# Performance work log

Hardware: AMD Instinct MI355X
Metric: run time of the kernel (lower is better)

The kernel has to match this reference:

```python
import jax, jax.numpy as jnp
import numpy as np

D_MODEL = 1024
D_STATE = 16
D_CONV = 4
EXPAND = 2
DT_RANK = 64
D_INNER = EXPAND * D_MODEL
B, L = 1, 2048


def setup_inputs() -> dict:
    key = jax.random.key(0)
    ks = jax.random.split(key, 10)
    x = jax.random.normal(ks[0], (B, L, D_MODEL), dtype=jnp.float32)
    # linear weights (stored as [out, in], like torch)
    W_in = jax.random.normal(ks[1], (2 * D_INNER, D_MODEL), dtype=jnp.float32) * (1.0 / np.sqrt(D_MODEL))
    conv_w = jax.random.normal(ks[2], (D_INNER, 1, D_CONV), dtype=jnp.float32) * (1.0 / np.sqrt(D_CONV))
    conv_b = jax.random.normal(ks[3], (D_INNER,), dtype=jnp.float32) * 0.02
    W_x = jax.random.normal(ks[4], (DT_RANK + 2 * D_STATE, D_INNER), dtype=jnp.float32) * (1.0 / np.sqrt(D_INNER))
    W_dt = jax.random.normal(ks[5], (D_INNER, DT_RANK), dtype=jnp.float32) * (1.0 / np.sqrt(DT_RANK))
    # dt bias init: inverse-softplus of dt ~ LogUniform(1e-3, 0.1)
    dt = jnp.exp(jax.random.uniform(ks[6], (D_INNER,)) * (np.log(0.1) - np.log(0.001)) + np.log(0.001))
    dt = jnp.clip(dt, 1e-4, None)
    b_dt = dt + jnp.log(-jnp.expm1(-dt))
    # A_log init: log(1..d_state) broadcast over d_inner
    A_log = jnp.log(jnp.broadcast_to(jnp.arange(1, D_STATE + 1, dtype=jnp.float32)[None, :], (D_INNER, D_STATE)))
    D_param = jnp.ones((D_INNER,), dtype=jnp.float32)
    W_out = jax.random.normal(ks[7], (D_MODEL, D_INNER), dtype=jnp.float32) * (1.0 / np.sqrt(D_INNER))
    return dict(x=x, W_in=W_in, conv_w=conv_w, conv_b=conv_b, W_x=W_x,
                W_dt=W_dt, b_dt=b_dt, A_log=A_log, D_param=D_param, W_out=W_out)


def _silu(v):
    return v * jax.nn.sigmoid(v)


def _mamba_forward(x, W_in, conv_w, conv_b, W_x, W_dt, b_dt, A_log, D_param, W_out):
    # in_proj: (B, L, 2*d_inner)
    xz = jnp.einsum('bld,ed->ble', x, W_in)
    x_in, z = jnp.split(xz, 2, axis=-1)  # each (B, L, d_inner)

    # depthwise causal conv1d (torch pads d_conv-1 both sides then truncates -> causal left pad)
    xc = jnp.transpose(x_in, (0, 2, 1))  # (B, d_inner, L)
    xc = jax.lax.conv_general_dilated(
        xc, conv_w,
        window_strides=(1,), padding=[(D_CONV - 1, 0)],
        dimension_numbers=('NCH', 'OIH', 'NCH'),
        feature_group_count=D_INNER)
    xc = xc + conv_b[None, :, None]
    x_conv = _silu(jnp.transpose(xc, (0, 2, 1)))  # (B, L, d_inner)

    # selective SSM
    A = -jnp.exp(A_log)  # (d_inner, d_state)
    x_dbl = jnp.einsum('bld,ed->ble', x_conv, W_x)  # (B, L, dt_rank + 2*d_state)
    dt_low, B_ssm, C = jnp.split(x_dbl, [DT_RANK, DT_RANK + D_STATE], axis=-1)
    dt = jax.nn.softplus(jnp.einsum('blr,dr->bld', dt_low, W_dt) + b_dt)  # (B, L, d_inner)

    dA = jnp.exp(jnp.einsum('bld,dn->bldn', dt, A))                        # (B, L, d_inner, d_state)
    dBx = dt[..., None] * B_ssm[:, :, None, :] * x_conv[..., None]          # dB * x, (B, L, d_inner, d_state)

    def step(h, inp):
        dA_t, dBx_t, C_t = inp          # (B, d, n), (B, d, n), (B, n)
        h = dA_t * h + dBx_t
        y_t = jnp.einsum('bdn,bn->bd', h, C_t)
        return h, y_t

    h0 = jnp.zeros((x.shape[0], D_INNER, D_STATE), dtype=x.dtype)
    xs = (jnp.swapaxes(dA, 0, 1), jnp.swapaxes(dBx, 0, 1), jnp.swapaxes(C, 0, 1))
    _, ys = jax.lax.scan(step, h0, xs)   # ys: (L, B, d_inner)
    y = jnp.swapaxes(ys, 0, 1) + x_conv * D_param  # (B, L, d_inner)

    y = y * _silu(z)
    return jnp.einsum('bld,ed->ble', y, W_out)  # (B, L, d_model)


def reference(x, W_in, conv_w, conv_b, W_x, W_dt, b_dt, A_log, D_param, W_out):
    return _mamba_forward(x, W_in, conv_w, conv_b, W_x, W_dt, b_dt, A_log, D_param, W_out)
```

## Files before the change

### kernel.cpp

```cpp
#include <hip/hip_runtime.h>
#include <math.h>

#define LSEQ   2048
#define DMODEL 1024
#define DINNER 2048
#define DSTATE 16
#define DTRANK 64
#define XCOLS  96
#define CL     32
#define NC     (LSEQ/CL)
#define SSTATE (DINNER*DSTATE)

typedef __attribute__((ext_vector_type(8))) short bf16x8;
typedef __attribute__((ext_vector_type(4))) float f32x4;
typedef unsigned short ushort_t;
typedef unsigned int uint_t;

__device__ __forceinline__ float siluf(float v) { return v / (1.f + __expf(-v)); }

__device__ __forceinline__ ushort_t f2bf(float f) {
    uint_t u = __float_as_uint(f);
    u += 0x7FFFu + ((u >> 16) & 1u);
    return (ushort_t)(u >> 16);
}
__device__ __forceinline__ float bf2f(ushort_t u) {
    return __uint_as_float((uint_t)u << 16);
}

__device__ __forceinline__ bf16x8 cvt8(float4 lo, float4 hi) {
    bf16x8 r;
    r[0] = (short)f2bf(lo.x); r[1] = (short)f2bf(lo.y);
    r[2] = (short)f2bf(lo.z); r[3] = (short)f2bf(lo.w);
    r[4] = (short)f2bf(hi.x); r[5] = (short)f2bf(hi.y);
    r[6] = (short)f2bf(hi.z); r[7] = (short)f2bf(hi.w);
    return r;
}

__global__ __launch_bounds__(256)
void cast6_kernel(const float* __restrict__ s0, ushort_t* __restrict__ d0, int c0,
                  const float* __restrict__ s1, ushort_t* __restrict__ d1, int c1,
                  const float* __restrict__ s2, ushort_t* __restrict__ d2, int c2,
                  const float* __restrict__ s3, ushort_t* __restrict__ d3, int c3,
                  const float* __restrict__ s4, ushort_t* __restrict__ d4, int c4,
                  float* __restrict__ z0, int cz)
{
    int i = (blockIdx.x * 256 + threadIdx.x) * 8;
    int tot = c0 + c1 + c2 + c3 + c4;
    if (i < tot) {
        const float* s; ushort_t* d;
        if (i < c0)                { s = s0 + i;                  d = d0 + i; }
        else if (i < c0+c1)        { s = s1 + (i-c0);             d = d1 + (i-c0); }
        else if (i < c0+c1+c2)     { s = s2 + (i-c0-c1);          d = d2 + (i-c0-c1); }
        else if (i < c0+c1+c2+c3)  { s = s3 + (i-c0-c1-c2);       d = d3 + (i-c0-c1-c2); }
        else                       { s = s4 + (i-c0-c1-c2-c3);    d = d4 + (i-c0-c1-c2-c3); }
        *(bf16x8*)d = cvt8(*(const float4*)s, *(const float4*)(s + 4));
    } else if (i < tot + cz) {
        float* z = z0 + (i - tot);
        *(float4*)z       = make_float4(0.f, 0.f, 0.f, 0.f);
        *(float4*)(z + 4) = make_float4(0.f, 0.f, 0.f, 0.f);
    }
}

__device__ __forceinline__ void stage_tile(const ushort_t* __restrict__ A,
                                           const ushort_t* __restrict__ B,
                                           ushort_t* As, ushort_t* Bs,
                                           int m0, int n0, int K, int k0, int tid)
{
#pragma unroll
    for (int j = 0; j < 2; j++) {
        const int c   = j * 256 + tid;
        const int row = c & 127;
        const int kbi = c >> 7;
        __builtin_amdgcn_global_load_lds(
            (const __attribute__((address_space(1))) uint_t*)(A + (size_t)(m0 + row) * K + k0 + kbi * 8),
            (__attribute__((address_space(3))) uint_t*)((char*)As + c * 16), 16, 0, 0);
        __builtin_amdgcn_global_load_lds(
            (const __attribute__((address_space(1))) uint_t*)(B + (size_t)(n0 + row) * K + k0 + kbi * 8),
            (__attribute__((address_space(3))) uint_t*)((char*)Bs + c * 16), 16, 0, 0);
    }
}

template<int EPI, int SPLITK>
__global__ __launch_bounds__(256)
void gemm_bf16(const ushort_t* __restrict__ A,
               const ushort_t* __restrict__ B,
               float* __restrict__ C,
               ushort_t* __restrict__ Xb,
               ushort_t* __restrict__ Gz,
               int M, int N, int K, size_t partStride)
{
    __shared__ ushort_t As[2][4096];
    __shared__ ushort_t Bs[2][4096];

    const int tid  = threadIdx.x;
    const int wid  = tid >> 6;
    const int lane = tid & 63;
    const int m0 = blockIdx.x * 128;
    const int n0 = blockIdx.y * 128;
    const int kcnt  = K / SPLITK;
    const int kbase = (SPLITK > 1) ? blockIdx.z * kcnt : 0;
    const int NT = kcnt / 32;
    float* Cp = (EPI == 0) ? C + (size_t)blockIdx.z * partStride : C;
    const int wr = (wid >> 1) * 64;
    const int wc = (wid & 1) * 64;
    const int lr = lane & 15;
    const int kbq = lane >> 4;

    f32x4 acc[4][4];
#pragma unroll
    for (int m = 0; m < 4; m++)
#pragma unroll
        for (int n = 0; n < 4; n++)
            acc[m][n] = (f32x4){0.f, 0.f, 0.f, 0.f};

    stage_tile(A, B, As[0], Bs[0], m0, n0, K, kbase, tid);

    for (int t = 0; t < NT; t++) {
        const int cur = t & 1;
        if (t + 1 < NT) {
            stage_tile(A, B, As[cur ^ 1], Bs[cur ^ 1], m0, n0, K, kbase + (t + 1) * 32, tid);
            asm volatile("s_waitcnt vmcnt(4)" ::: "memory");
        } else {
            asm volatile("s_waitcnt vmcnt(0)" ::: "memory");
        }
        __builtin_amdgcn_s_barrier();
        __builtin_amdgcn_sched_barrier(0);

        bf16x8 af[4], bfr[4];
#pragma unroll
        for (int m = 0; m < 4; m++)
            af[m] = *(const bf16x8*)&As[cur][(kbq * 128 + wr + m * 16 + lr) * 8];
#pragma unroll
        for (int n = 0; n < 4; n++)
            bfr[n] = *(const bf16x8*)&Bs[cur][(kbq * 128 + wc + n * 16 + lr) * 8];
#pragma unroll
        for (int m = 0; m < 4; m++)
#pragma unroll
            for (int n = 0; n < 4; n++)
                acc[m][n] = __builtin_amdgcn_mfma_f32_16x16x32_bf16(af[m], bfr[n], acc[m][n], 0, 0, 0);

        __builtin_amdgcn_sched_barrier(0);
        __builtin_amdgcn_s_barrier();
    }

    const int er = (lane >> 4) * 4;
    const int ec = lane & 15;
    if (EPI == 0) {
#pragma unroll
        for (int m = 0; m < 4; m++) {
            const int grow = m0 + wr + m * 16 + er;
#pragma unroll
            for (int n = 0; n < 4; n++) {
                const int gcol = n0 + wc + n * 16 + ec;
#pragma unroll
                for (int r = 0; r < 4; r++)
                    Cp[(size_t)(grow + r) * N + gcol] = acc[m][n][r];
            }
        }
    } else {
        const bool xside = (n0 < DINNER);
        ushort_t* eps = (wid < 2) ? As[wid] : Bs[wid - 2];
#pragma unroll
        for (int m = 0; m < 4; m++)
#pragma unroll
            for (int n = 0; n < 4; n++)
#pragma unroll
                for (int r = 0; r < 4; r++) {
                    const int rl = m * 16 + er + r;
                    const int cl = n * 16 + ec;
                    float v = acc[m][n][r];
                    eps[rl * 64 + (cl ^ ((rl & 7) * 8))] =
                        xside ? f2bf(v) : f2bf(siluf(v));
                }
        __syncthreads();
        const int row8 = lane >> 3;
        const int c8   = (lane & 7) * 8;
#pragma unroll
        for (int p = 0; p < 8; p++) {
            const int rl = p * 8 + row8;
            bf16x8 v = *(const bf16x8*)&eps[rl * 64 + (c8 ^ ((rl & 7) * 8))];
            const int grow = m0 + wr + rl;
            const int gcol = n0 + wc + c8;
            if (xside)
                *(bf16x8*)(Xb + (size_t)grow * DINNER + gcol) = v;
            else
                *(bf16x8*)(Gz + (size_t)grow * DINNER + (gcol - DINNER)) = v;
        }
    }
}

__global__ __launch_bounds__(256)
void add2_kernel(const float* __restrict__ p0, const float* __restrict__ p1,
                 float* __restrict__ out, int n)
{
    int i = (blockIdx.x * 256 + threadIdx.x) * 4;
    if (i >= n) return;
    float4 a = *(const float4*)(p0 + i);
    float4 b = *(const float4*)(p1 + i);
    *(float4*)(out + i) = make_float4(a.x + b.x, a.y + b.y, a.z + b.z, a.w + b.w);
}

__global__ __launch_bounds__(256)
void gemm_xdbl(const ushort_t* __restrict__ A,
               const ushort_t* __restrict__ B,
               float* __restrict__ Cout)
{
    const int tid = threadIdx.x, wid = tid >> 6, lane = tid & 63;
    const int m0 = blockIdx.x * 128;
    const int kbase = blockIdx.z * 128;
    const int wr = (wid >> 1) * 64;
    const int wc = (wid & 1) * 48;
    const int lr = lane & 15;
    const int kq = (lane >> 4) * 8;

    f32x4 acc[4][3];
#pragma unroll
    for (int m = 0; m < 4; m++)
#pragma unroll
        for (int n = 0; n < 3; n++)
            acc[m][n] = (f32x4){0.f, 0.f, 0.f, 0.f};

#pragma unroll
    for (int ks = 0; ks < 4; ks++) {
        const int k0 = kbase + ks * 32;
        bf16x8 af[4], bfr[3];
#pragma unroll
        for (int m = 0; m < 4; m++)
            af[m] = *(const bf16x8*)(A + (size_t)(m0 + wr + m * 16 + lr) * DINNER + k0 + kq);
#pragma unroll
        for (int n = 0; n < 3; n++)
            bfr[n] = *(const bf16x8*)(B + (size_t)(wc + n * 16 + lr) * DINNER + k0 + kq);
#pragma unroll
        for (int m = 0; m < 4; m++)
#pragma unroll
            for (int n = 0; n < 3; n++)
                acc[m][n] = __builtin_amdgcn_mfma_f32_16x16x32_bf16(af[m], bfr[n], acc[m][n], 0, 0, 0);
    }

    const int er = (lane >> 4) * 4;
    const int ec = lane & 15;
#pragma unroll
    for (int m = 0; m < 4; m++)
#pragma unroll
        for (int n = 0; n < 3; n++)
#pragma unroll
            for (int r = 0; r < 4; r++)
                atomicAdd(&Cout[(size_t)(m0 + wr + m * 16 + er + r) * XCOLS + wc + n * 16 + ec],
                          acc[m][n][r]);
}

__global__ __launch_bounds__(256)
void gemm_dt(const float* __restrict__ Axd,
             const ushort_t* __restrict__ Bw,
             const float* __restrict__ bias,
             ushort_t* __restrict__ dtmb)
{
    __shared__ ushort_t eps4[4][4096];
    const int tid = threadIdx.x, wid = tid >> 6, lane = tid & 63;
    const int m0 = blockIdx.x * 128;
    const int n0 = blockIdx.y * 128;
    const int wr = (wid >> 1) * 64;
    const int wc = (wid & 1) * 64;
    const int lr = lane & 15;
    const int kq = (lane >> 4) * 8;

    f32x4 acc[4][4];
#pragma unroll
    for (int m = 0; m < 4; m++)
#pragma unroll
        for (int n = 0; n < 4; n++)
            acc[m][n] = (f32x4){0.f, 0.f, 0.f, 0.f};

#pragma unroll
    for (int kk = 0; kk < 2; kk++) {
        bf16x8 af[4], bfr[4];
#pragma unroll
        for (int m = 0; m < 4; m++) {
            const float* p = Axd + (size_t)(m0 + wr + m * 16 + lr) * XCOLS + kk * 32 + kq;
            af[m] = cvt8(*(const float4*)p, *(const float4*)(p + 4));
        }
#pragma unroll
        for (int n = 0; n < 4; n++)
            bfr[n] = *(const bf16x8*)(Bw + (size_t)(n0 + wc + n * 16 + lr) * DTRANK + kk * 32 + kq);
#pragma unroll
        for (int m = 0; m < 4; m++)
#pragma unroll
            for (int n = 0; n < 4; n++)
                acc[m][n] = __builtin_amdgcn_mfma_f32_16x16x32_bf16(af[m], bfr[n], acc[m][n], 0, 0, 0);
    }

    const int er = (lane >> 4) * 4;
    const int ec = lane & 15;
    ushort_t* eps = eps4[wid];
#pragma unroll
    for (int m = 0; m < 4; m++)
#pragma unroll
        for (int n = 0; n < 4; n++) {
            const int cl = n * 16 + ec;
            const float bv = bias[n0 + wc + cl];
#pragma unroll
            for (int r = 0; r < 4; r++) {
                const int rl = m * 16 + er + r;
                float c = acc[m][n][r] + bv;
                c = (c > 20.f) ? c : log1pf(__expf(c));
                eps[rl * 64 + (cl ^ ((rl & 7) * 8))] = f2bf(c);
            }
        }
    __syncthreads();
    const int row8 = lane >> 3;
    const int c8   = (lane & 7) * 8;
#pragma unroll
    for (int p = 0; p < 8; p++) {
        const int rl = p * 8 + row8;
        bf16x8 v = *(const bf16x8*)&eps[rl * 64 + (c8 ^ ((rl & 7) * 8))];
        dtmb[(size_t)(m0 + wr + rl) * DINNER + n0 + wc + c8] = 0;
        *(bf16x8*)(dtmb + (size_t)(m0 + wr + rl) * DINNER + n0 + wc + c8) = v;
    }
}

__global__ __launch_bounds__(256)
void conv_silu_kernel(const ushort_t* __restrict__ xinb,
                      const float* __restrict__ conv_w,
                      const float* __restrict__ conv_b,
                      ushort_t* __restrict__ xcb)
{
    int idx = blockIdx.x * 256 + threadIdx.x;
    if (idx >= LSEQ * DINNER) return;
    int t = idx / DINNER;
    int d = idx - t * DINNER;
    float acc = conv_b[d];
#pragma unroll
    for (int j = 0; j < 4; j++) {
        int tt = t - 3 + j;
        if (tt >= 0)
            acc = fmaf(conv_w[d*4 + j], bf2f(xinb[(size_t)tt * DINNER + d]), acc);
    }
    xcb[idx] = f2bf(siluf(acc));
}

__global__ __launch_bounds__(256)
void scan_phase1(const ushort_t* __restrict__ dtmb,
                 const float* __restrict__ xdbl,
                 const ushort_t* __restrict__ xcb,
                 const float* __restrict__ A_log,
                 float2* __restrict__ state)
{
    __shared__ float Bs[CL][16];
    const int tid = threadIdx.x;
    const int d = blockIdx.x * 256 + tid;
    const int c = blockIdx.y;
    const int t0 = c * CL;

    {
        int t = tid >> 3, n = (tid * 2) & 15;
        float2 v = *(const float2*)&xdbl[(size_t)(t0 + t) * XCOLS + DTRANK + n];
        Bs[t][n] = v.x; Bs[t][n + 1] = v.y;
    }

    float a[16];
#pragma unroll
    for (int q = 0; q < 4; q++) {
        f32x4 v = *(const f32x4*)&A_log[(size_t)d * DSTATE + q * 4];
#pragma unroll
        for (int j = 0; j < 4; j++) a[q * 4 + j] = -__expf(v[j]);
    }
    float h[16];
#pragma unroll
    for (int n = 0; n < 16; n++) h[n] = 0.f;
    float sdt = 0.f;

    __syncthreads();

    float dtv = bf2f(dtmb[(size_t)t0 * DINNER + d]);
    float xv  = bf2f(xcb[(size_t)t0 * DINNER + d]);
    for (int tt = 0; tt < CL; tt++) {
        int tn_ = t0 + ((tt + 1 < CL) ? tt + 1 : tt);
        float dtv_n = bf2f(dtmb[(size_t)tn_ * DINNER + d]);
        float xv_n  = bf2f(xcb[(size_t)tn_ * DINNER + d]);

        f32x4 Bq[4];
#pragma unroll
        for (int q = 0; q < 4; q++) Bq[q] = *(const f32x4*)&Bs[tt][q * 4];
        float dtx = dtv * xv;
        sdt += dtv;
#pragma unroll
        for (int n = 0; n < 16; n++) {
            float e = __expf(dtv * a[n]);
            h[n] = fmaf(e, h[n], dtx * Bq[n >> 2][n & 3]);
        }
        dtv = dtv_n; xv = xv_n;
    }

#pragma unroll
    for (int n = 0; n < 16; n++)
        state[(size_t)c * SSTATE + (size_t)n * DINNER + d] =
            make_float2(__expf(a[n] * sdt), h[n]);
}

__global__ __launch_bounds__(256)
void scan_phase2(float2* __restrict__ state)
{
    const int idx = blockIdx.x * 256 + threadIdx.x;
    float carry = 0.f;
#pragma unroll
    for (int c = 0; c < NC; c++) {
        float2 s = state[(size_t)c * SSTATE + idx];
        ((float*)&state[(size_t)c * SSTATE + idx])[1] = carry;
        carry = fmaf(s.x, carry, s.y);
    }
}

__global__ __launch_bounds__(256)
void scan_phase3(const ushort_t* __restrict__ dtmb,
                 const float* __restrict__ xdbl,
                 const ushort_t* __restrict__ xcb,
                 const float* __restrict__ A_log,
                 const float* __restrict__ Dp,
                 const ushort_t* __restrict__ gz,
                 const float2* __restrict__ state,
                 ushort_t* __restrict__ yb)
{
    __shared__ float Bs[CL][16];
    __shared__ float Cs[CL][16];
    const int tid = threadIdx.x;
    const int d = blockIdx.x * 256 + tid;
    const int c = blockIdx.y;
    const int t0 = c * CL;

    {
        int r = tid & 127;
        int t = r >> 2, n = (r * 4) & 15;
        const float* src = &xdbl[(size_t)(t0 + t) * XCOLS + DTRANK + ((tid < 128) ? 0 : DSTATE) + n];
        float4 v = *(const float4*)src;
        float* dst = (tid < 128) ? &Bs[t][n] : &Cs[t][n];
        dst[0] = v.x; dst[1] = v.y; dst[2] = v.z; dst[3] = v.w;
    }

    float a[16];
#pragma unroll
    for (int q = 0; q < 4; q++) {
        f32x4 v = *(const f32x4*)&A_log[(size_t)d * DSTATE + q * 4];
#pragma unroll
        for (int j = 0; j < 4; j++) a[q * 4 + j] = -__expf(v[j]);
    }
    const float Dv = Dp[d];
    float h[16];
#pragma unroll
    for (int n = 0; n < 16; n++)
        h[n] = state[(size_t)c * SSTATE + (size_t)n * DINNER + d].y;

    __syncthreads();

    float dtv = bf2f(dtmb[(size_t)t0 * DINNER + d]);
    float xv  = bf2f(xcb[(size_t)t0 * DINNER + d]);
    for (int tt = 0; tt < CL; tt++) {
        const int t = t0 + tt;
        int tn_ = t0 + ((tt + 1 < CL) ? tt + 1 : tt);
        float dtv_n = bf2f(dtmb[(size_t)tn_ * DINNER + d]);
        float xv_n  = bf2f(xcb[(size_t)tn_ * DINNER + d]);
        float gzv   = bf2f(gz[(size_t)t * DINNER + d]);

        f32x4 Bq[4], Cq[4];
#pragma unroll
        for (int q = 0; q < 4; q++) {
            Bq[q] = *(const f32x4*)&Bs[tt][q * 4];
            Cq[q] = *(const f32x4*)&Cs[tt][q * 4];
        }
        float dtx = dtv * xv;
        float y = 0.f;
#pragma unroll
        for (int n = 0; n < 16; n++) {
            float e = __expf(dtv * a[n]);
            h[n] = fmaf(e, h[n], dtx * Bq[n >> 2][n & 3]);
            y = fmaf(h[n], Cq[n >> 2][n & 3], y);
        }
        yb[(size_t)t * DINNER + d] = f2bf((y + Dv * xv) * gzv);
        dtv = dtv_n; xv = xv_n;
    }
}

extern "C" void kernel_launch(void* const* d_in, const int* in_sizes, int n_in,
                              void* d_out, int out_size, void* d_ws, size_t ws_size,
                              hipStream_t stream)
{
    const float* x      = (const float*)d_in[0];
    const float* W_in   = (const float*)d_in[1];
    const float* conv_w = (const float*)d_in[2];
    const float* conv_b = (const float*)d_in[3];
    const float* W_x    = (const float*)d_in[4];
    const float* W_dt   = (const float*)d_in[5];
    const float* b_dt   = (const float*)d_in[6];
    const float* A_log  = (const float*)d_in[7];
    const float* D_par  = (const float*)d_in[8];
    const float* W_out  = (const float*)d_in[9];
    float* out = (float*)d_out;
    float* ws  = (float*)d_ws;

    float*  xdbl  = ws;
    float2* state = (float2*)(xdbl + (size_t)LSEQ * XCOLS);
    ushort_t* xb   = (ushort_t*)(state + (size_t)NC * SSTATE);
    ushort_t* Wib  = xb   + (size_t)LSEQ * DMODEL;
    ushort_t* Wob  = Wib  + (size_t)(2*DINNER) * DMODEL;
    ushort_t* Wxb  = Wob  + (size_t)DMODEL * DINNER;
    ushort_t* Wdtb = Wxb  + (size_t)XCOLS * DINNER;
    ushort_t* xinb = Wdtb + (size_t)DINNER * DTRANK;
    ushort_t* gz   = xinb + (size_t)LSEQ * DINNER;
    ushort_t* xcb  = gz   + (size_t)LSEQ * DINNER;
    ushort_t* dtmb = xcb  + (size_t)LSEQ * DINNER;
    ushort_t* yb   = dtmb + (size_t)LSEQ * DINNER;
    float* outp = (float*)xinb;

    {
        int c0 = LSEQ * DMODEL, c1 = 2 * DINNER * DMODEL, c2 = DMODEL * DINNER;
        int c3 = XCOLS * DINNER, c4 = DINNER * DTRANK;
        int cz = LSEQ * XCOLS;
        int total = c0 + c1 + c2 + c3 + c4 + cz;
        hipLaunchKernelGGL(cast6_kernel, dim3((total / 8 + 255) / 256), dim3(256), 0, stream,
                           x, xb, c0, W_in, Wib, c1, W_out, Wob, c2,
                           W_x, Wxb, c3, W_dt, Wdtb, c4, xdbl, cz);
    }

    hipLaunchKernelGGL((gemm_bf16<1,1>), dim3(LSEQ/128, (2*DINNER)/128), dim3(256), 0, stream,
                       xb, Wib, (float*)nullptr, xinb, gz, LSEQ, 2*DINNER, DMODEL, (size_t)0);

    hipLaunchKernelGGL(conv_silu_kernel, dim3((LSEQ*DINNER)/256), dim3(256), 0, stream,
                       xinb, conv_w, conv_b, xcb);

    hipLaunchKernelGGL(gemm_xdbl, dim3(LSEQ/128, 1, 16), dim3(256), 0, stream,
                       xcb, Wxb, xdbl);

    hipLaunchKernelGGL(gemm_dt, dim3(LSEQ/128, DINNER/128), dim3(256), 0, stream,
                       xdbl, Wdtb, b_dt, dtmb);

    hipLaunchKernelGGL(scan_phase1, dim3(DINNER/256, NC), dim3(256), 0, stream,
                       dtmb, xdbl, xcb, A_log, state);
    hipLaunchKernelGGL(scan_phase2, dim3(SSTATE/256), dim3(256), 0, stream,
                       state);
    hipLaunchKernelGGL(scan_phase3, dim3(DINNER/256, NC), dim3(256), 0, stream,
                       dtmb, xdbl, xcb, A_log, D_par, gz, state, yb);

    hipLaunchKernelGGL((gemm_bf16<0,2>), dim3(LSEQ/128, DMODEL/128, 2), dim3(256), 0, stream,
                       yb, Wob, outp, (ushort_t*)nullptr, (ushort_t*)nullptr,
                       LSEQ, DMODEL, DINNER, (size_t)(LSEQ*DMODEL));
    hipLaunchKernelGGL(add2_kernel, dim3((LSEQ*DMODEL/4)/256), dim3(256), 0, stream,
                       outp, outp + (size_t)LSEQ*DMODEL, out, LSEQ*DMODEL);
}
```

Measured before the change: 203.3 us.

## Use 256x256-tile 512-thread GEMM for in_proj and drop redundant dt store

```diff
diff --git a/kernel.cpp b/kernel.cpp
--- a/kernel.cpp
+++ b/kernel.cpp
@@ -61,6 +61,120 @@
     }
 }
 
+__device__ __forceinline__ void stage256(const ushort_t* __restrict__ A,
+                                         const ushort_t* __restrict__ B,
+                                         ushort_t* LDS, int buf,
+                                         int m0, int n0, int k0, int tid)
+{
+    ushort_t* As = LDS + buf * 16384;
+    ushort_t* Bs = LDS + 32768 + buf * 16384;
+#pragma unroll
+    for (int j = 0; j < 4; j++) {
+        const int c   = j * 512 + tid;
+        const int row = c & 255;
+        const int kb  = c >> 8;
+        __builtin_amdgcn_global_load_lds(
+            (const __attribute__((address_space(1))) uint_t*)(A + (size_t)(m0 + row) * DMODEL + k0 + kb * 8),
+            (__attribute__((address_space(3))) uint_t*)((char*)As + c * 16), 16, 0, 0);
+        __builtin_amdgcn_global_load_lds(
+            (const __attribute__((address_space(1))) uint_t*)(B + (size_t)(n0 + row) * DMODEL + k0 + kb * 8),
+            (__attribute__((address_space(3))) uint_t*)((char*)Bs + c * 16), 16, 0, 0);
+    }
+}
+
+__global__ __launch_bounds__(512)
+void gemm256_inproj(const ushort_t* __restrict__ A,
+                    const ushort_t* __restrict__ B,
+                    ushort_t* __restrict__ Xb,
+                    ushort_t* __restrict__ Gz)
+{
+    __shared__ ushort_t LDS[65536];
+
+    const int tid  = threadIdx.x;
+    const int wid  = tid >> 6;
+    const int lane = tid & 63;
+    const int m0 = blockIdx.x * 256;
+    const int n0 = blockIdx.y * 256;
+    const int NT = DMODEL / 64;
+    const int wr = (wid >> 2) * 128;
+    const int wc = (wid & 3) * 64;
+    const int lr = lane & 15;
+    const int kq = lane >> 4;
+
+    f32x4 acc[8][4];
+#pragma unroll
+    for (int m = 0; m < 8; m++)
+#pragma unroll
+        for (int n = 0; n < 4; n++)
+            acc[m][n] = (f32x4){0.f, 0.f, 0.f, 0.f};
+
+    stage256(A, B, LDS, 0, m0, n0, 0, tid);
+
+    for (int t = 0; t < NT; t++) {
+        const int cur = t & 1;
+        if (t + 1 < NT) {
+            stage256(A, B, LDS, cur ^ 1, m0, n0, (t + 1) * 64, tid);
+            asm volatile("s_waitcnt vmcnt(8)" ::: "memory");
+        } else {
+            asm volatile("s_waitcnt vmcnt(0)" ::: "memory");
+        }
+        __builtin_amdgcn_s_barrier();
+        __builtin_amdgcn_sched_barrier(0);
+
+        const ushort_t* Asc = LDS + cur * 16384;
+        const ushort_t* Bsc = LDS + 32768 + cur * 16384;
+
+        bf16x8 bfr[2][4];
+#pragma unroll
+        for (int kk = 0; kk < 2; kk++)
+#pragma unroll
+            for (int n = 0; n < 4; n++)
+                bfr[kk][n] = *(const bf16x8*)&Bsc[((kk * 4 + kq) * 256 + wc + n * 16 + lr) * 8];
+#pragma unroll
+        for (int m = 0; m < 8; m++) {
+            bf16x8 af0 = *(const bf16x8*)&Asc[((0 * 4 + kq) * 256 + wr + m * 16 + lr) * 8];
+            bf16x8 af1 = *(const bf16x8*)&Asc[((1 * 4 + kq) * 256 + wr + m * 16 + lr) * 8];
+#pragma unroll
+            for (int n = 0; n < 4; n++) {
+                acc[m][n] = __builtin_amdgcn_mfma_f32_16x16x32_bf16(af0, bfr[0][n], acc[m][n], 0, 0, 0);
+                acc[m][n] = __builtin_amdgcn_mfma_f32_16x16x32_bf16(af1, bfr[1][n], acc[m][n], 0, 0, 0);
+            }
+        }
+
+        __builtin_amdgcn_sched_barrier(0);
+        __builtin_amdgcn_s_barrier();
+    }
+
+    const bool xside = (n0 < DINNER);
+    ushort_t* eps = LDS + wid * 8192;
+    const int er = (lane >> 4) * 4;
+    const int ec = lane & 15;
+#pragma unroll
+    for (int m = 0; m < 8; m++)
+#pragma unroll
+        for (int n = 0; n < 4; n++)
+#pragma unroll
+            for (int r = 0; r < 4; r++) {
+                const int rl = m * 16 + er + r;
+                const int cl = n * 16 + ec;
+                float v = acc[m][n][r];
+                eps[rl * 64 + (cl ^ ((rl & 7) * 8))] = xside ? f2bf(v) : f2bf(siluf(v));
+            }
+    const int row8 = lane >> 3;
+    const int c8   = (lane & 7) * 8;
+#pragma unroll
+    for (int p = 0; p < 16; p++) {
+        const int rl = p * 8 + row8;
+        bf16x8 v = *(const bf16x8*)&eps[rl * 64 + (c8 ^ ((rl & 7) * 8))];
+        const int grow = m0 + wr + rl;
+        const int gcol = n0 + wc + c8;
+        if (xside)
+            *(bf16x8*)(Xb + (size_t)grow * DINNER + gcol) = v;
+        else
+            *(bf16x8*)(Gz + (size_t)grow * DINNER + (gcol - DINNER)) = v;
+    }
+}
+
 __device__ __forceinline__ void stage_tile(const ushort_t* __restrict__ A,
                                            const ushort_t* __restrict__ B,
                                            ushort_t* As, ushort_t* Bs,
@@ -80,13 +194,11 @@
     }
 }
 
-template<int EPI, int SPLITK>
+template<int SPLITK>
 __global__ __launch_bounds__(256)
 void gemm_bf16(const ushort_t* __restrict__ A,
                const ushort_t* __restrict__ B,
                float* __restrict__ C,
-               ushort_t* __restrict__ Xb,
-               ushort_t* __restrict__ Gz,
                int M, int N, int K, size_t partStride)
 {
     __shared__ ushort_t As[2][4096];
@@ -100,7 +212,7 @@
     const int kcnt  = K / SPLITK;
     const int kbase = (SPLITK > 1) ? blockIdx.z * kcnt : 0;
     const int NT = kcnt / 32;
-    float* Cp = (EPI == 0) ? C + (size_t)blockIdx.z * partStride : C;
+    float* Cp = C + (size_t)blockIdx.z * partStride;
     const int wr = (wid >> 1) * 64;
     const int wc = (wid & 1) * 64;
     const int lr = lane & 15;
@@ -145,46 +257,15 @@
 
     const int er = (lane >> 4) * 4;
     const int ec = lane & 15;
-    if (EPI == 0) {
-#pragma unroll
-        for (int m = 0; m < 4; m++) {
-            const int grow = m0 + wr + m * 16 + er;
-#pragma unroll
-            for (int n = 0; n < 4; n++) {
-                const int gcol = n0 + wc + n * 16 + ec;
-#pragma unroll
-                for (int r = 0; r < 4; r++)
-                    Cp[(size_t)(grow + r) * N + gcol] = acc[m][n][r];
-            }
-        }
-    } else {
-        const bool xside = (n0 < DINNER);
-        ushort_t* eps = (wid < 2) ? As[wid] : Bs[wid - 2];
-#pragma unroll
-        for (int m = 0; m < 4; m++)
-#pragma unroll
-            for (int n = 0; n < 4; n++)
-#pragma unroll
-                for (int r = 0; r < 4; r++) {
-                    const int rl = m * 16 + er + r;
-                    const int cl = n * 16 + ec;
-                    float v = acc[m][n][r];
-                    eps[rl * 64 + (cl ^ ((rl & 7) * 8))] =
-                        xside ? f2bf(v) : f2bf(siluf(v));
-                }
-        __syncthreads();
-        const int row8 = lane >> 3;
-        const int c8   = (lane & 7) * 8;
-#pragma unroll
-        for (int p = 0; p < 8; p++) {
-            const int rl = p * 8 + row8;
-            bf16x8 v = *(const bf16x8*)&eps[rl * 64 + (c8 ^ ((rl & 7) * 8))];
-            const int grow = m0 + wr + rl;
-            const int gcol = n0 + wc + c8;
-            if (xside)
-                *(bf16x8*)(Xb + (size_t)grow * DINNER + gcol) = v;
-            else
-                *(bf16x8*)(Gz + (size_t)grow * DINNER + (gcol - DINNER)) = v;
+#pragma unroll
+    for (int m = 0; m < 4; m++) {
+        const int grow = m0 + wr + m * 16 + er;
+#pragma unroll
+        for (int n = 0; n < 4; n++) {
+            const int gcol = n0 + wc + n * 16 + ec;
+#pragma unroll
+            for (int r = 0; r < 4; r++)
+                Cp[(size_t)(grow + r) * N + gcol] = acc[m][n][r];
         }
     }
 }
@@ -313,7 +394,6 @@
     for (int p = 0; p < 8; p++) {
         const int rl = p * 8 + row8;
         bf16x8 v = *(const bf16x8*)&eps[rl * 64 + (c8 ^ ((rl & 7) * 8))];
-        dtmb[(size_t)(m0 + wr + rl) * DINNER + n0 + wc + c8] = 0;
         *(bf16x8*)(dtmb + (size_t)(m0 + wr + rl) * DINNER + n0 + wc + c8) = v;
     }
 }
@@ -520,8 +600,8 @@
                            W_x, Wxb, c3, W_dt, Wdtb, c4, xdbl, cz);
     }
 
-    hipLaunchKernelGGL((gemm_bf16<1,1>), dim3(LSEQ/128, (2*DINNER)/128), dim3(256), 0, stream,
-                       xb, Wib, (float*)nullptr, xinb, gz, LSEQ, 2*DINNER, DMODEL, (size_t)0);
+    hipLaunchKernelGGL(gemm256_inproj, dim3(LSEQ/256, (2*DINNER)/256), dim3(512), 0, stream,
+                       xb, Wib, xinb, gz);
 
     hipLaunchKernelGGL(conv_silu_kernel, dim3((LSEQ*DINNER)/256), dim3(256), 0, stream,
                        xinb, conv_w, conv_b, xcb);
@@ -539,9 +619,8 @@
     hipLaunchKernelGGL(scan_phase3, dim3(DINNER/256, NC), dim3(256), 0, stream,
                        dtmb, xdbl, xcb, A_log, D_par, gz, state, yb);
 
-    hipLaunchKernelGGL((gemm_bf16<0,2>), dim3(LSEQ/128, DMODEL/128, 2), dim3(256), 0, stream,
-                       yb, Wob, outp, (ushort_t*)nullptr, (ushort_t*)nullptr,
-                       LSEQ, DMODEL, DINNER, (size_t)(LSEQ*DMODEL));
+    hipLaunchKernelGGL((gemm_bf16<2>), dim3(LSEQ/128, DMODEL/128, 2), dim3(256), 0, stream,
+                       yb, Wob, outp, LSEQ, DMODEL, DINNER, (size_t)(LSEQ*DMODEL));
     hipLaunchKernelGGL(add2_kernel, dim3((LSEQ*DMODEL/4)/256), dim3(256), 0, stream,
                        outp, outp + (size_t)LSEQ*DMODEL, out, LSEQ*DMODEL);
 }
```

Result: slower. 223.8 us (+10.1%).
